# Kernel optimization log

Hardware: AMD Instinct MI355X
Metric: run time of the kernel (lower is better)

The kernel has to match this reference:

```python
import jax, jax.numpy as jnp
import numpy as np

# static config (mirrors init_kwargs)
FS = 512          # frame_seqlen
NFPB = 2          # num_frame_per_block
NIB = 3           # num image/action/state blocks
NAPB = 32         # num_action_per_block
NSPB = 1          # num_state_per_block
LOCAL = 4         # local_attn_size (frames)
FIRST = FS
IMGB = NIB * NFPB * FS
ALEN = NIB * NAPB
SLEN = NIB * NSPB
TOTAL = FIRST + IMGB + ALEN + SLEN   # 3683
DIM = 1536
NH = 12
HD = DIM // NH    # 128
EPS = 1e-6


def _build_mask():
    # faithful port of _visualize_attention_mask (the block-sparse pattern)
    m = np.zeros((TOTAL, TOTAL), dtype=bool)
    fi0, fi1 = 0, FIRST
    ib0, ib1 = fi1, fi1 + IMGB
    a0, a1 = ib1, ib1 + ALEN
    s0 = a1
    m[fi0:fi1, fi0:fi1] = True  # first image: self only (sink)
    for b in range(NIB):
        bs = ib0 + b * NFPB * FS
        be = ib0 + (b + 1) * NFPB * FS
        m[bs:be, fi0:fi1] = True                      # sink
        kv = max(ib0, be - LOCAL * FS)                # local window
        m[bs:be, kv:be] = True
        m[bs:be, a0 + b * NAPB:a0 + (b + 1) * NAPB] = True
        m[bs:be, s0 + b * NSPB:s0 + (b + 1) * NSPB] = True
    for b in range(NIB):
        ab0 = a0 + b * NAPB
        ab1 = a0 + (b + 1) * NAPB
        m[ab0:ab1, fi0:fi1] = True
        ibe = ib0 + (b + 1) * NFPB * FS
        kv = max(ib0, ibe - LOCAL * FS)
        m[ab0:ab1, kv:ibe] = True
        m[ab0:ab1, ab0:ab1] = True
        m[ab0:ab1, s0 + b * NSPB:s0 + (b + 1) * NSPB] = True
    for b in range(NIB):
        ss = s0 + b * NSPB
        se = s0 + (b + 1) * NSPB
        m[ss:se, ss:se] = True
    return m

_MASK = jnp.asarray(_build_mask())


def _rms_norm(x, g):
    # WanRMSNorm over full dim, fp32 accumulation
    v = jnp.mean(jnp.square(x.astype(jnp.float32)), axis=-1, keepdims=True)
    return (x.astype(jnp.float32) * jax.lax.rsqrt(v + EPS)).astype(x.dtype) * g


def _rope(x, cos, sin):
    # x: [B,L,n,hd]; pairs are consecutive (..., hd//2, 2)
    B, L, n, d = x.shape
    xp = x.reshape(B, L, n, d // 2, 2)
    xr, xi = xp[..., 0], xp[..., 1]
    c = cos[None, :, None, :]
    s = sin[None, :, None, :]
    yr = xr * c - xi * s
    yi = xr * s + xi * c
    return jnp.stack([yr, yi], axis=-1).reshape(B, L, n, d)


def setup_inputs() -> dict:
    key = jax.random.key(0)
    ks = jax.random.split(key, 16)
    x = jax.random.normal(ks[0], (1, TOTAL, DIM), jnp.float32)

    def mkfreq(k, L):
        ang = jax.random.uniform(k, (L, HD // 2), jnp.float32, 0.0, 2.0 * np.pi)
        return jnp.stack([jnp.cos(ang), jnp.sin(ang)], axis=-1).reshape(L, HD)

    freqs = mkfreq(ks[1], FIRST + IMGB)
    freqs_action = mkfreq(ks[2], ALEN)
    freqs_state = mkfreq(ks[3], SLEN)
    sc = 1.0 / np.sqrt(DIM)
    Wq = jax.random.normal(ks[4], (DIM, DIM), jnp.float32) * sc
    Wk = jax.random.normal(ks[5], (DIM, DIM), jnp.float32) * sc
    Wv = jax.random.normal(ks[6], (DIM, DIM), jnp.float32) * sc
    Wo = jax.random.normal(ks[7], (DIM, DIM), jnp.float32) * sc
    bq = jax.random.normal(ks[8], (DIM,), jnp.float32) * 0.01
    bk = jax.random.normal(ks[9], (DIM,), jnp.float32) * 0.01
    bv = jax.random.normal(ks[10], (DIM,), jnp.float32) * 0.01
    bo = jax.random.normal(ks[11], (DIM,), jnp.float32) * 0.01
    gq = jnp.ones((DIM,), jnp.float32)
    gk = jnp.ones((DIM,), jnp.float32)
    return {"x": x, "freqs": freqs, "freqs_action": freqs_action,
            "freqs_state": freqs_state, "Wq": Wq, "bq": bq, "Wk": Wk, "bk": bk,
            "Wv": Wv, "bv": bv, "Wo": Wo, "bo": bo, "gq": gq, "gk": gk}


def reference(x, freqs, freqs_action, freqs_state, Wq, bq, Wk, bk, Wv, bv, Wo, bo, gq, gk):
    B, L, _ = x.shape
    q = _rms_norm(x @ Wq + bq, gq).reshape(B, L, NH, HD)
    k = _rms_norm(x @ Wk + bk, gk).reshape(B, L, NH, HD)
    v = (x @ Wv + bv).reshape(B, L, NH, HD)
    # full-sequence rope: image freqs then action freqs then state freqs
    f = jnp.concatenate([freqs, freqs_action, freqs_state], axis=0).reshape(L, HD // 2, 2)
    cos, sin = f[..., 0], f[..., 1]
    q = _rope(q, cos, sin)
    k = _rope(k, cos, sin)
    scores = jnp.einsum('bqnd,bknd->bnqk', q, k) / np.sqrt(HD)
    scores = jnp.where(_MASK[None, None], scores, jnp.finfo(scores.dtype).min)
    p = jax.nn.softmax(scores, axis=-1)
    o = jnp.einsum('bnqk,bknd->bqnd', p, v).reshape(B, L, DIM)
    return o @ Wo + bo
```

## Files before the change

kernel.cpp:

```cpp
#include <hip/hip_runtime.h>

#define LSEQ 3683
#define LPAD 3840
#define DIMSZ 1536
#define NHEAD 12
#define HEADD 128
#define SM_SCALE 0.088388347648318447f

typedef unsigned short u16;
typedef unsigned int u32;
typedef __bf16 bf16x8 __attribute__((ext_vector_type(8)));
typedef float f32x4 __attribute__((ext_vector_type(4)));

__device__ __forceinline__ u16 f2b(float f) {
  u32 u = __float_as_uint(f);
  u += 0x7FFFu + ((u >> 16) & 1u);
  return (u16)(u >> 16);
}
__device__ __forceinline__ float b2f(u16 s) {
  return __uint_as_float(((u32)s) << 16);
}
__device__ __forceinline__ int imax(int a, int b) { return a > b ? a : b; }

__device__ __forceinline__ void gl_lds16(const u16* g, u16* l) {
  __builtin_amdgcn_global_load_lds((const __attribute__((address_space(1))) u32*)g,
                                   (__attribute__((address_space(3))) u32*)l,
                                   16, 0, 0);
}

__device__ __forceinline__ int xcd_swz(int orig, int nwg) {
  int q = nwg >> 3, r = nwg & 7;
  int x = orig & 7, l = orig >> 3;
  return (x < r ? x * (q + 1) : r * (q + 1) + (x - r) * q) + l;
}

__global__ void convert_x_kernel(const float* __restrict__ x, u16* __restrict__ xb) {
  long idx = (long)blockIdx.x * blockDim.x + threadIdx.x;
  long base = idx * 4;
  if (base >= (long)LPAD * DIMSZ) return;
  float4 v;
  if (base < (long)LSEQ * DIMSZ) v = *(const float4*)(x + base);
  else v = make_float4(0.f, 0.f, 0.f, 0.f);
  ushort4 o;
  o.x = f2b(v.x); o.y = f2b(v.y); o.z = f2b(v.z); o.w = f2b(v.w);
  *(ushort4*)(xb + base) = o;
}

__global__ void transpose_w_kernel(const float* __restrict__ W0, const float* __restrict__ W1,
                                   const float* __restrict__ W2, const float* __restrict__ W3,
                                   u16* __restrict__ Wt) {
  const float* W = (blockIdx.z == 0) ? W0 : (blockIdx.z == 1) ? W1 : (blockIdx.z == 2) ? W2 : W3;
  u16* dst = Wt + (size_t)blockIdx.z * DIMSZ * DIMSZ;
  __shared__ float tile[32][33];
  int k0 = blockIdx.x * 32, n0 = blockIdx.y * 32;
  int tx = threadIdx.x & 31, ty = threadIdx.x >> 5;
  #pragma unroll
  for (int i = 0; i < 4; i++) {
    int k = k0 + ty + i * 8;
    tile[ty + i * 8][tx] = W[(size_t)k * DIMSZ + n0 + tx];
  }
  __syncthreads();
  #pragma unroll
  for (int i = 0; i < 4; i++) {
    int n = n0 + ty + i * 8;
    dst[(size_t)n * DIMSZ + k0 + tx] = f2b(tile[tx][ty + i * 8]);
  }
}

#define BAR() __builtin_amdgcn_s_barrier()
#define LGK0() asm volatile("s_waitcnt lgkmcnt(0)" ::: "memory")
#define LGK8() asm volatile("s_waitcnt lgkmcnt(8)" ::: "memory")
#define VMC9() asm volatile("s_waitcnt vmcnt(9)" ::: "memory")
#define VMC6() asm volatile("s_waitcnt vmcnt(6)" ::: "memory")
#define VMC0() asm volatile("s_waitcnt vmcnt(0)" ::: "memory")
#define PRIO1() __builtin_amdgcn_s_setprio(1)
#define PRIO0() __builtin_amdgcn_s_setprio(0)

#define STG_A(buf, q, kt) \
  gl_lds16(gA + (size_t)((q) * 64) * DIMSZ + (kt), &Asg[buf][((q) * 64 + w * 8) * 64]);
#define STG_B(buf, q, kt) \
  gl_lds16(gB + (size_t)((q) * 64) * DIMSZ + (kt), &Bsg[buf][((q) * 64 + w * 8) * 64]);

#define LDA3(buf, mh) { \
  _Pragma("unroll") for (int mf = 0; mf < 3; mf++) { \
    int rb = (wm * 96 + (mh) * 48 + mf * 16) * 64; \
    Ar[mf * 2 + 0] = *(const bf16x8*)&Asg[buf][rb + off0]; \
    Ar[mf * 2 + 1] = *(const bf16x8*)&Asg[buf][rb + off1]; } }
#define LDB3(buf, nh) { \
  _Pragma("unroll") for (int nf = 0; nf < 3; nf++) { \
    int rb = (wn * 96 + (nh) * 48 + nf * 16) * 64; \
    Br[nh][nf * 2 + 0] = *(const bf16x8*)&Bsg[buf][rb + off0]; \
    Br[nh][nf * 2 + 1] = *(const bf16x8*)&Bsg[buf][rb + off1]; } }

#define MFMAQ3(mh, nh) { \
  _Pragma("unroll") for (int mf = 0; mf < 3; mf++) \
    _Pragma("unroll") for (int nf = 0; nf < 3; nf++) { \
      acc[(mh)*3+mf][(nh)*3+nf] = __builtin_amdgcn_mfma_f32_16x16x32_bf16(Ar[mf*2+0], Br[nh][nf*2+0], acc[(mh)*3+mf][(nh)*3+nf], 0, 0, 0); \
      acc[(mh)*3+mf][(nh)*3+nf] = __builtin_amdgcn_mfma_f32_16x16x32_bf16(Ar[mf*2+1], Br[nh][nf*2+1], acc[(mh)*3+mf][(nh)*3+nf], 0, 0, 0); } }

__launch_bounds__(512, 2)
__global__ void gemm_qkv384_kernel(const u16* __restrict__ A, const u16* __restrict__ Wt,
                                   const float* __restrict__ bq, const float* __restrict__ bk,
                                   const float* __restrict__ bv,
                                   u16* __restrict__ Qb, u16* __restrict__ Kb,
                                   u16* __restrict__ Vt) {
  __shared__ __align__(16) u16 Asg[2][384 * 64];
  __shared__ __align__(16) u16 Bsg[2][192 * 64];

  int wg = xcd_swz(blockIdx.x, 10 * 24);
  int nt = wg % 24;
  int m0 = (wg / 24) * 384;
  int which = nt >> 3;
  const float* bias = (which == 0) ? bq : (which == 1) ? bk : bv;

  int t = threadIdx.x;
  int lane = t & 63, w = t >> 6;
  int c = lane & 15, g = lane >> 4;
  int wm = w >> 1, wn = w & 1;

  int srow = t >> 3;
  int schunk = ((t & 7) ^ (srow & 7)) * 8;
  const u16* gA = A + (size_t)(m0 + srow) * DIMSZ + schunk;
  const u16* gB = Wt + (size_t)(nt * 192 + srow) * DIMSZ + schunk;

  int off0 = c * 64 + ((g) ^ (c & 7)) * 8;
  int off1 = c * 64 + ((g + 4) ^ (c & 7)) * 8;

  f32x4 acc[6][6];
  f32x4 zero = {0.f, 0.f, 0.f, 0.f};
  #pragma unroll
  for (int am = 0; am < 6; am++)
    #pragma unroll
    for (int an = 0; an < 6; an++) acc[am][an] = zero;
  bf16x8 Ar[6];
  bf16x8 Br[2][6];

  STG_B(0, 0, 0) STG_B(0, 1, 0) STG_B(0, 2, 0)
  STG_A(0, 0, 0) STG_A(0, 1, 0) STG_A(0, 2, 0)
  STG_A(0, 3, 0) STG_A(0, 4, 0) STG_A(0, 5, 0)
  STG_B(1, 0, 64) STG_B(1, 1, 64) STG_B(1, 2, 64)
  STG_A(1, 0, 64) STG_A(1, 1, 64) STG_A(1, 2, 64)
  STG_A(1, 3, 64) STG_A(1, 4, 64) STG_A(1, 5, 64)
  VMC9();
  BAR();

  for (int i = 0; i < DIMSZ / 64 / 2 - 1; ++i) {
    int kt2 = (2 * i + 2) * 64;
    int kt3 = (2 * i + 3) * 64;
    LDA3(0, 0) LDB3(0, 0)
    LGK8(); BAR(); LGK0();
    PRIO1(); MFMAQ3(0, 0) PRIO0();
    BAR();
    LDB3(0, 1)
    BAR(); LGK0();
    PRIO1(); MFMAQ3(0, 1) PRIO0();
    BAR();
    LDA3(0, 1)
    STG_B(0, 0, kt2) STG_B(0, 1, kt2) STG_B(0, 2, kt2)
    BAR(); LGK0();
    PRIO1(); MFMAQ3(1, 1) PRIO0();
    BAR();
    STG_A(0, 0, kt2) STG_A(0, 1, kt2) STG_A(0, 2, kt2)
    VMC6(); BAR();
    PRIO1(); MFMAQ3(1, 0) PRIO0();
    BAR();
    LDA3(1, 0) LDB3(1, 0)
    STG_A(0, 3, kt2) STG_A(0, 4, kt2) STG_A(0, 5, kt2)
    LGK8(); BAR(); LGK0();
    PRIO1(); MFMAQ3(0, 0) PRIO0();
    BAR();
    LDB3(1, 1)
    BAR(); LGK0();
    PRIO1(); MFMAQ3(0, 1) PRIO0();
    BAR();
    LDA3(1, 1)
    STG_B(1, 0, kt3) STG_B(1, 1, kt3) STG_B(1, 2, kt3)
    BAR(); LGK0();
    PRIO1(); MFMAQ3(1, 1) PRIO0();
    BAR();
    STG_A(1, 0, kt3) STG_A(1, 1, kt3) STG_A(1, 2, kt3)
    STG_A(1, 3, kt3) STG_A(1, 4, kt3) STG_A(1, 5, kt3)
    VMC9(); BAR();
    PRIO1(); MFMAQ3(1, 0) PRIO0();
    BAR();
  }

  {
    LDA3(0, 0) LDB3(0, 0)
    LGK8(); BAR(); LGK0();
    PRIO1(); MFMAQ3(0, 0) PRIO0();
    BAR();
    LDB3(0, 1)
    BAR(); LGK0();
    PRIO1(); MFMAQ3(0, 1) PRIO0();
    BAR();
    LDA3(0, 1)
    BAR(); LGK0();
    PRIO1(); MFMAQ3(1, 1) PRIO0();
    BAR();
    VMC0(); BAR();
    PRIO1(); MFMAQ3(1, 0) PRIO0();
    BAR();
    LDA3(1, 0) LDB3(1, 0)
    LGK8(); BAR(); LGK0();
    PRIO1(); MFMAQ3(0, 0) PRIO0();
    BAR();
    LDB3(1, 1)
    BAR(); LGK0();
    PRIO1(); MFMAQ3(0, 1) PRIO0();
    BAR();
    LDA3(1, 1)
    BAR(); LGK0();
    PRIO1(); MFMAQ3(1, 1) PRIO0();
    MFMAQ3(1, 0)
  }

  #pragma unroll
  for (int an = 0; an < 6; an++) {
    int ncol = (nt & 7) * 192 + wn * 96 + (an / 3) * 48 + (an % 3) * 16 + c;
    float bvv = bias[ncol];
    #pragma unroll
    for (int am = 0; am < 6; am++) {
      int rowb = m0 + wm * 96 + (am / 3) * 48 + (am % 3) * 16 + 4 * g;
      if (which == 2) {
        ushort4 pv;
        pv.x = f2b(acc[am][an][0] + bvv);
        pv.y = f2b(acc[am][an][1] + bvv);
        pv.z = f2b(acc[am][an][2] + bvv);
        pv.w = f2b(acc[am][an][3] + bvv);
        *(ushort4*)&Vt[(size_t)ncol * LPAD + rowb] = pv;
      } else {
        u16* P = (which == 1) ? Kb : Qb;
        #pragma unroll
        for (int r = 0; r < 4; r++)
          P[(size_t)(rowb + r) * DIMSZ + ncol] = f2b(acc[am][an][r] + bvv);
      }
    }
  }
}

#define GEMM_PROLOGUE()                                                          \
  __shared__ __align__(16) u16 As[4][128 * 32];                                  \
  __shared__ __align__(16) u16 Bs[4][128 * 32];                                  \
  int t = threadIdx.x;                                                           \
  int lane = t & 63, w = t >> 6;                                                 \
  int g = lane >> 4, c = lane & 15;                                              \
  int wm = w >> 1, wn = w & 1;                                                   \
  f32x4 acc[4][4];                                                               \
  f32x4 zero = {0.f, 0.f, 0.f, 0.f};                                             \
  _Pragma("unroll") for (int fr = 0; fr < 4; fr++)                               \
      _Pragma("unroll") for (int fc = 0; fc < 4; fc++) acc[fr][fc] = zero;       \
  int srcc = (((lane & 3) ^ ((lane >> 2) & 3))) * 8;    \
  const u16* gA = A + (size_t)(m0 + w * 32 + (lane >> 2)) * DIMSZ + srcc;        \
  const u16* gB = Bt + (size_t)(n0 + w * 32 + (lane >> 2)) * DIMSZ + srcc;       \
  int gsw = (g ^ (c & 3)) * 8;

#define GEMM_STAGE(buf, kt)                                                      \
  _Pragma("unroll") for (int q = 0; q < 2; q++) {                                \
    gl_lds16(gA + (size_t)(q * 16) * DIMSZ + (kt), &As[buf][(w * 32 + q * 16) * 32]); \
    gl_lds16(gB + (size_t)(q * 16) * DIMSZ + (kt), &Bs[buf][(w * 32 + q * 16) * 32]); \
  }

#define GEMM_COMPUTE(buf)                                                        \
  {                                                                              \
    bf16x8 af[4], bfr[4];                                                        \
    _Pragma("unroll") for (int fr = 0; fr < 4; fr++)                             \
        af[fr] = *(const bf16x8*)&As[buf][(wm * 64 + fr * 16 + c) * 32 + gsw];   \
    _Pragma("unroll") for (int fc = 0; fc < 4; fc++)                             \
        bfr[fc] = *(const bf16x8*)&Bs[buf][(wn * 64 + fc * 16 + c) * 32 + gsw];  \
    _Pragma("unroll") for (int fr = 0; fr < 4; fr++)                             \
        _Pragma("unroll") for (int fc = 0; fc < 4; fc++)                         \
            acc[fr][fc] = __builtin_amdgcn_mfma_f32_16x16x32_bf16(af[fr], bfr[fc], acc[fr][fc], 0, 0, 0); \
  }

#define GEMM_MAINLOOP()                                                          \
  GEMM_STAGE(0, 0)                                                               \
  GEMM_STAGE(1, 32)                                                              \
  GEMM_STAGE(2, 64)                                                              \
  {                                                                              \
    const int nk = DIMSZ / 32;                                                   \
    for (int ki = 0; ki < nk; ki++) {                                            \
      int rem = nk - ki;                                                         \
      if (rem > 2)      asm volatile("s_waitcnt vmcnt(8)" ::: "memory");         \
      else if (rem == 2) asm volatile("s_waitcnt vmcnt(4)" ::: "memory");        \
      else               asm volatile("s_waitcnt vmcnt(0)" ::: "memory");        \
      __builtin_amdgcn_s_barrier();                                              \
      if (ki + 3 < nk) { GEMM_STAGE((ki + 3) & 3, (ki + 3) * 32) }               \
      GEMM_COMPUTE(ki & 3)                                                       \
    }                                                                            \
  }

__launch_bounds__(256)
__global__ void gemm_out_kernel(const u16* __restrict__ A, const u16* __restrict__ Bt,
                                const float* __restrict__ bias, float* __restrict__ outF) {
  int wg = xcd_swz(blockIdx.x, 29 * 12);
  int n0 = (wg % 12) * 128;
  int m0 = (wg / 12) * 128;

  GEMM_PROLOGUE()
  GEMM_MAINLOOP()

  #pragma unroll
  for (int fc = 0; fc < 4; fc++) {
    int col = n0 + wn * 64 + fc * 16 + c;
    float bvv = bias[col];
    #pragma unroll
    for (int fr = 0; fr < 4; fr++) {
      int rowb = m0 + wm * 64 + fr * 16 + 4 * g;
      #pragma unroll
      for (int r = 0; r < 4; r++) {
        int row = rowb + r;
        if (row < LSEQ) outF[(size_t)row * DIMSZ + col] = acc[fr][fc][r] + bvv;
      }
    }
  }
}

__launch_bounds__(256)
__global__ void normrope_kernel(u16* __restrict__ Qb, u16* __restrict__ Kb,
                                const float* __restrict__ gq, const float* __restrict__ gk,
                                const float* __restrict__ freqs, const float* __restrict__ freqs_a,
                                const float* __restrict__ freqs_s) {
  int l = blockIdx.x;
  int sel = blockIdx.y;
  u16* P = sel ? Kb : Qb;
  const float* gvec = sel ? gk : gq;
  int t = threadIdx.x;
  u16* row = P + (size_t)l * DIMSZ;
  float xv[6];
  #pragma unroll
  for (int i = 0; i < 3; i++) {
    int p = i * 256 + t;
    ushort2 u = *(const ushort2*)(row + 2 * p);
    xv[2 * i] = b2f(u.x);
    xv[2 * i + 1] = b2f(u.y);
  }
  float ss = 0.f;
  #pragma unroll
  for (int i = 0; i < 6; i++) ss += xv[i] * xv[i];
  #pragma unroll
  for (int d = 32; d; d >>= 1) ss += __shfl_down(ss, d);
  __shared__ float red[4];
  __shared__ float rshare;
  if ((t & 63) == 0) red[t >> 6] = ss;
  __syncthreads();
  if (t == 0) rshare = rsqrtf((red[0] + red[1] + red[2] + red[3]) * (1.0f / DIMSZ) + 1e-6f);
  __syncthreads();
  float rms = rshare;

  const float* f = (l < 3584) ? (freqs + (size_t)l * HEADD)
                : (l < 3680) ? (freqs_a + (size_t)(l - 3584) * HEADD)
                             : (freqs_s + (size_t)(l - 3680) * HEADD);
  #pragma unroll
  for (int i = 0; i < 3; i++) {
    int p = i * 256 + t;
    int j = p & 63;
    float2 csn = *(const float2*)(f + 2 * j);
    float2 gv = *(const float2*)(gvec + 2 * p);
    float xr = xv[2 * i] * rms * gv.x;
    float xi = xv[2 * i + 1] * rms * gv.y;
    ushort2 o;
    o.x = f2b(xr * csn.x - xi * csn.y);
    o.y = f2b(xr * csn.y + xi * csn.x);
    *(ushort2*)(row + 2 * p) = o;
  }
}

#define PSLOT_U16 16640
__launch_bounds__(256, 2)
__global__ void attn_dense_kernel(const u16* __restrict__ Q, const u16* __restrict__ K,
                                  const u16* __restrict__ Vt, u16* __restrict__ O,
                                  u16* __restrict__ DP) {
  __shared__ __align__(16) u16 Ks[2][32 * 144];
  __shared__ __align__(16) u16 Vs[2][128 * 40];
  __shared__ __align__(16) u16 Pl[4][32 * 40];

  int bx = blockIdx.x;
  int qbase, h, part, nparts, fb;
  if (bx < 48) { qbase = (bx / 12) * 128; h = bx % 12; part = 0; nparts = 1; fb = -1; }
  else if (bx < 336) { int i = bx - 48; int qb = i / 36; h = (i / 3) % 12; part = i % 3; nparts = 3; fb = 0; qbase = 512 + qb * 128; }
  else if (bx < 720) { int i = bx - 336; int qb = i / 48; h = (i / 4) % 12; part = i % 4; nparts = 4; fb = 1; qbase = 1536 + qb * 128; }
  else { int i = bx - 720; int qb = i / 48; h = (i / 4) % 12; part = i % 4; nparts = 4; fb = 2; qbase = 2560 + qb * 128; }

  int S0, E0, S1, E1, S2, E2, S3, E3, niv;
  if (fb < 0) { S0 = 0; E0 = 512; S1 = E1 = S2 = E2 = S3 = E3 = 0; niv = 1; }
  else {
    int be = 512 + (fb + 1) * 1024;
    int kv = imax(512, be - 2048);
    S0 = 0; E0 = 512; S1 = kv; E1 = be;
    S2 = 3584 + 32 * fb; E2 = S2 + 32; S3 = 3680 + fb; E3 = S3 + 1; niv = 4;
  }
  int B0 = S0 & ~31, B1 = S1 & ~31, B2 = S2 & ~31, B3 = S3 & ~31;
  int T1 = (E0 - B0 + 31) >> 5;
  int T2 = T1 + ((niv > 1) ? ((E1 - B1 + 31) >> 5) : 0);
  int T3 = T2 + ((niv > 2) ? ((E2 - B2 + 31) >> 5) : 0);
  int T4 = T3 + ((niv > 3) ? ((E3 - B3 + 31) >> 5) : 0);
  int ntile = T4;
  int rlo = (ntile * part) / nparts, rhi = (ntile * (part + 1)) / nparts;

  auto tile_of = [&](int f, int& k0, int& lo, int& hi) {
    k0 = B0 + (f << 5); lo = S0; hi = E0;
    if (niv > 1 && f >= T1) { k0 = B1 + ((f - T1) << 5); lo = S1; hi = E1; }
    if (niv > 2 && f >= T2) { k0 = B2 + ((f - T2) << 5); lo = S2; hi = E2; }
    if (niv > 3 && f >= T3) { k0 = B3 + ((f - T3) << 5); lo = S3; hi = E3; }
  };

  int T = threadIdx.x;
  int lane = T & 63, w = T >> 6, g = lane >> 4, c = lane & 15;

  const u16* kgp = K + (size_t)(T >> 3) * DIMSZ + h * HEADD + 8 * (T & 7);
  int kds = (T >> 3) * 144 + 8 * (T & 7);
  const u16* vgp = Vt + ((size_t)h * HEADD + (T >> 1)) * LPAD + 16 * (T & 1);
  int vds = (T >> 1) * 40 + 16 * (T & 1);

  uint4 sk0, sk1, sv0, sv1;
  auto stage_load = [&](int k0) {
    const u16* kp = kgp + (size_t)k0 * DIMSZ;
    sk0 = *(const uint4*)(kp);
    sk1 = *(const uint4*)(kp + 64);
    sv0 = *(const uint4*)(vgp + k0);
    sv1 = *(const uint4*)(vgp + k0 + 8);
  };
  auto stage_write = [&](int buf) {
    *(uint4*)&Ks[buf][kds] = sk0;
    *(uint4*)&Ks[buf][kds + 64] = sk1;
    *(uint4*)&Vs[buf][vds] = sv0;
    *(uint4*)&Vs[buf][vds + 8] = sv1;
  };

  int qrow0 = qbase + 32 * w;
  bf16x8 qf[2][4];
  #pragma unroll
  for (int a = 0; a < 2; a++) {
    const u16* qp = Q + (size_t)(qrow0 + a * 16 + c) * DIMSZ + h * HEADD + 8 * g;
    #pragma unroll
    for (int s = 0; s < 4; s++) qf[a][s] = *(const bf16x8*)(qp + 32 * s);
  }

  f32x4 zero = {0.f, 0.f, 0.f, 0.f};
  f32x4 acc[2][8];
  f32x4 lacc[2];
  #pragma unroll
  for (int a = 0; a < 2; a++) {
    lacc[a] = zero;
    #pragma unroll
    for (int cc = 0; cc < 8; cc++) acc[a][cc] = zero;
  }
  bf16x8 onesv;
  {
    u16 ob = 0x3F80;
    #pragma unroll
    for (int i = 0; i < 8; i++) onesv[i] = ((const __bf16*)&ob)[0];
  }

  u16* Pw = &Pl[w][0];
  const float c1 = SM_SCALE * 1.44269504088896340f;
  const float c2 = 12.0f * 1.44269504088896340f;

  {
    int k0, lo, hi; tile_of(rlo, k0, lo, hi);
    stage_load(k0);
    stage_write(0);
  }
  __syncthreads();
  int cur = 0;

  for (int t = rlo; t < rhi; ++t) {
    int ck0, clo, chi; tile_of(t, ck0, clo, chi);
    bool pre = (t + 1 < rhi);
    if (pre) { int nk0, nl, nh; tile_of(t + 1, nk0, nl, nh); stage_load(nk0); }

    f32x4 sc[2][2];
    sc[0][0] = zero; sc[0][1] = zero; sc[1][0] = zero; sc[1][1] = zero;
    #pragma unroll
    for (int k2 = 0; k2 < 2; k2++)
      #pragma unroll
      for (int s = 0; s < 4; s++) {
        bf16x8 kf = *(const bf16x8*)&Ks[cur][(16 * k2 + c) * 144 + 32 * s + 8 * g];
        sc[0][k2] = __builtin_amdgcn_mfma_f32_16x16x32_bf16(qf[0][s], kf, sc[0][k2], 0, 0, 0);
        sc[1][k2] = __builtin_amdgcn_mfma_f32_16x16x32_bf16(qf[1][s], kf, sc[1][k2], 0, 0, 0);
      }

    #pragma unroll
    for (int a = 0; a < 2; a++)
      #pragma unroll
      for (int k2 = 0; k2 < 2; k2++) {
        int k = ck0 + k2 * 16 + c;
        bool valid = (k >= clo) && (k < chi);
        #pragma unroll
        for (int r = 0; r < 4; r++) {
          float p = exp2f(sc[a][k2][r] * c1 - c2);
          Pw[(a * 16 + 4 * g + r) * 40 + k2 * 16 + c] = valid ? f2b(p) : (u16)0;
        }
      }
    asm volatile("s_waitcnt lgkmcnt(0)" ::: "memory");
    __builtin_amdgcn_sched_barrier(0);

    bf16x8 pa0 = *(const bf16x8*)&Pw[c * 40 + 8 * g];
    bf16x8 pa1 = *(const bf16x8*)&Pw[(16 + c) * 40 + 8 * g];

    #pragma unroll
    for (int cc = 0; cc < 8; cc++) {
      bf16x8 vf = *(const bf16x8*)&Vs[cur][(cc * 16 + c) * 40 + 8 * g];
      acc[0][cc] = __builtin_amdgcn_mfma_f32_16x16x32_bf16(pa0, vf, acc[0][cc], 0, 0, 0);
      acc[1][cc] = __builtin_amdgcn_mfma_f32_16x16x32_bf16(pa1, vf, acc[1][cc], 0, 0, 0);
    }
    lacc[0] = __builtin_amdgcn_mfma_f32_16x16x32_bf16(pa0, onesv, lacc[0], 0, 0, 0);
    lacc[1] = __builtin_amdgcn_mfma_f32_16x16x32_bf16(pa1, onesv, lacc[1], 0, 0, 0);

    if (pre) stage_write(cur ^ 1);
    __syncthreads();
    cur ^= 1;
  }

  if (nparts == 1) {
    float inv[2][4];
    #pragma unroll
    for (int a = 0; a < 2; a++)
      #pragma unroll
      for (int r = 0; r < 4; r++) inv[a][r] = (lacc[a][r] > 0.f) ? 1.0f / lacc[a][r] : 0.f;
    #pragma unroll
    for (int a = 0; a < 2; a++)
      #pragma unroll
      for (int cc = 0; cc < 8; cc++)
        #pragma unroll
        for (int r = 0; r < 4; r++) {
          int row = qrow0 + a * 16 + 4 * g + r;
          O[(size_t)row * DIMSZ + h * HEADD + cc * 16 + c] = f2b(acc[a][cc][r] * inv[a][r]);
        }
  } else {
    int qb = (qbase - 512 - fb * 1024) >> 7;
    int sbase = (fb == 0) ? 0 : (fb == 1 ? 288 : 672);
    int slot = sbase + (qb * 12 + h) * nparts + part;
    u16* DPs = DP + (size_t)slot * PSLOT_U16;
    float* lout = (float*)(DPs + 16384);
    #pragma unroll
    for (int a = 0; a < 2; a++) {
      #pragma unroll
      for (int cc = 0; cc < 8; cc++)
        #pragma unroll
        for (int r = 0; r < 4; r++)
          DPs[(32 * w + a * 16 + 4 * g + r) * 128 + cc * 16 + c] = f2b(acc[a][cc][r]);
      if (c == 0)
        #pragma unroll
        for (int r = 0; r < 4; r++) lout[32 * w + a * 16 + 4 * g + r] = lacc[a][r];
    }
  }
}

__launch_bounds__(256)
__global__ void attn_merge_dense(const u16* __restrict__ DP, u16* __restrict__ O) {
  int qi = blockIdx.x, h = blockIdx.y;
  int fb = qi >> 3, qb = qi & 7;
  int nparts = (fb == 0) ? 3 : 4;
  int sbase = (fb == 0) ? 0 : (fb == 1 ? 288 : 672);
  int slot0 = sbase + (qb * 12 + h) * nparts;
  int qbase = 512 + fb * 1024 + qb * 128;
  int T = threadIdx.x;
  int row = T >> 1, c0 = 64 * (T & 1);

  float sum[64];
  #pragma unroll
  for (int j = 0; j < 64; j++) sum[j] = 0.f;
  float l = 0.f;
  for (int p = 0; p < nparts; p++) {
    const u16* S = DP + (size_t)(slot0 + p) * PSLOT_U16;
    l += ((const float*)(S + 16384))[row];
    #pragma unroll
    for (int j = 0; j < 64; j += 8) {
      uint4 v = *(const uint4*)&S[row * 128 + c0 + j];
      const u16* pv = (const u16*)&v;
      #pragma unroll
      for (int q = 0; q < 8; q++) sum[j + q] += b2f(pv[q]);
    }
  }
  float inv = (l > 0.f) ? 1.0f / l : 0.f;
  u16 tmp[64];
  #pragma unroll
  for (int j = 0; j < 64; j++) tmp[j] = f2b(sum[j] * inv);
  u16* op = O + (size_t)(qbase + row) * DIMSZ + h * HEADD + c0;
  #pragma unroll
  for (int j = 0; j < 64; j += 8) *(uint4*)(op + j) = *(uint4*)&tmp[j];
}

__launch_bounds__(256, 2)
__global__ void attn_tail_kernel(const u16* __restrict__ Q, const u16* __restrict__ K,
                                 const u16* __restrict__ Vt, u16* __restrict__ O,
                                 float* __restrict__ Part) {
  __shared__ __align__(16) char smem[20608];
  __shared__ float Lsum[32];

  int bx = blockIdx.x;
  int h = blockIdx.y;
  int qt, part;
  if (bx < 3) { qt = 112 + bx; part = 0; }
  else if (bx < 6) { qt = 112 + (bx - 3); part = 1; }
  else { qt = 115; part = 0; }
  int qbase = qt * 32;
  bool heavy = (qt <= 114);

  int t = threadIdx.x, lane = t & 63, w = t >> 6, g = lane >> 4, c = lane & 15;

  int S0, E0, S1, E1, S2, E2, S3, E3, niv;
  if (qbase < 3680) {
    int b = (qbase - 3584) >> 5;
    int ibe = 512 + (b + 1) * 1024;
    int kv = imax(512, ibe - 2048);
    S0 = 0; E0 = 512; S1 = kv; E1 = ibe;
    S2 = 3584 + 32 * b; E2 = S2 + 32; S3 = 3680 + b; E3 = S3 + 1; niv = 4;
  } else {
    S0 = 3680; E0 = 3683; S1 = S2 = S3 = 0; E1 = E2 = E3 = 0; niv = 1;
  }
  bool diag = (qbase >= 3680);

  int B0 = S0 & ~31, B1 = S1 & ~31, B2 = S2 & ~31, B3 = S3 & ~31;
  int T1 = (E0 - B0 + 31) >> 5;
  int T2 = T1 + ((niv > 1) ? ((E1 - B1 + 31) >> 5) : 0);
  int T3 = T2 + ((niv > 2) ? ((E2 - B2 + 31) >> 5) : 0);
  int T4 = T3 + ((niv > 3) ? ((E3 - B3 + 31) >> 5) : 0);
  int ntile = T4;

  int rlo = 0, rhi = ntile;
  if (heavy) { int half = (ntile + 1) >> 1; if (part == 0) rhi = half; else rlo = half; }

  auto tile_of = [&](int f, int& k0, int& lo, int& hi) {
    k0 = B0 + (f << 5); lo = S0; hi = E0;
    if (niv > 1 && f >= T1) { k0 = B1 + ((f - T1) << 5); lo = S1; hi = E1; }
    if (niv > 2 && f >= T2) { k0 = B2 + ((f - T2) << 5); lo = S2; hi = E2; }
    if (niv > 3 && f >= T3) { k0 = B3 + ((f - T3) << 5); lo = S3; hi = E3; }
  };

  bf16x8 qf[2][4];
  #pragma unroll
  for (int a = 0; a < 2; a++) {
    const u16* qp = Q + (size_t)(qbase + a * 16 + c) * DIMSZ + h * HEADD + 8 * g;
    #pragma unroll
    for (int s = 0; s < 4; s++) qf[a][s] = *(const bf16x8*)(qp + 32 * s);
  }

  f32x4 zero = {0.f, 0.f, 0.f, 0.f};
  f32x4 acc[2][8];
  f32x4 lacc[2];
  #pragma unroll
  for (int a = 0; a < 2; a++) {
    lacc[a] = zero;
    #pragma unroll
    for (int cc = 0; cc < 8; cc++) acc[a][cc] = zero;
  }
  bf16x8 onesv;
  {
    u16 ob = 0x3F80;
    #pragma unroll
    for (int i = 0; i < 8; i++) onesv[i] = ((const __bf16*)&ob)[0];
  }

  u16* PwA = (u16*)smem + w * 2560;
  u16* PwB = PwA + 1280;

  bf16x8 kc[2][4], vbuf[8], pa0, pa1;
  const float c1 = SM_SCALE * 1.44269504088896340f;
  const float c2 = 12.0f * 1.44269504088896340f;

  auto loadK = [&](int k0) {
    #pragma unroll
    for (int k2 = 0; k2 < 2; k2++) {
      const u16* kp = K + (size_t)(k0 + 16 * k2 + c) * DIMSZ + h * HEADD + 8 * g;
      #pragma unroll
      for (int s = 0; s < 4; s++) kc[k2][s] = *(const bf16x8*)(kp + 32 * s);
    }
  };
  auto loadV = [&](int k0) {
    #pragma unroll
    for (int cc = 0; cc < 8; cc++)
      vbuf[cc] = *(const bf16x8*)(Vt + (size_t)(h * HEADD + cc * 16 + c) * LPAD + k0 + 8 * g);
  };
  auto QKf = [&](f32x4 (&sc)[2][2]) {
    sc[0][0] = zero; sc[0][1] = zero; sc[1][0] = zero; sc[1][1] = zero;
    #pragma unroll
    for (int k2 = 0; k2 < 2; k2++)
      #pragma unroll
      for (int s = 0; s < 4; s++) {
        sc[0][k2] = __builtin_amdgcn_mfma_f32_16x16x32_bf16(qf[0][s], kc[k2][s], sc[0][k2], 0, 0, 0);
        sc[1][k2] = __builtin_amdgcn_mfma_f32_16x16x32_bf16(qf[1][s], kc[k2][s], sc[1][k2], 0, 0, 0);
      }
  };
  auto smstore = [&](f32x4 (&sc)[2][2], int k0, int lo, int hi, u16* Pw) {
    #pragma unroll
    for (int a = 0; a < 2; a++)
      #pragma unroll
      for (int k2 = 0; k2 < 2; k2++) {
        int k = k0 + k2 * 16 + c;
        bool valid = (k >= lo) && (k < hi);
        #pragma unroll
        for (int r = 0; r < 4; r++) {
          float p = exp2f(sc[a][k2][r] * c1 - c2);
          bool v = valid;
          if (diag) { int qr = qbase + a * 16 + 4 * g + r; v = v && (k == qr); }
          Pw[(a * 16 + 4 * g + r) * 40 + k2 * 16 + c] = v ? f2b(p) : (u16)0;
        }
      }
  };
  auto readP = [&](u16* Pw) {
    pa0 = *(const bf16x8*)&Pw[c * 40 + 8 * g];
    pa1 = *(const bf16x8*)&Pw[(16 + c) * 40 + 8 * g];
  };
  auto PV = [&]() {
    #pragma unroll
    for (int cc = 0; cc < 8; cc++) {
      acc[0][cc] = __builtin_amdgcn_mfma_f32_16x16x32_bf16(pa0, vbuf[cc], acc[0][cc], 0, 0, 0);
      acc[1][cc] = __builtin_amdgcn_mfma_f32_16x16x32_bf16(pa1, vbuf[cc], acc[1][cc], 0, 0, 0);
    }
    lacc[0] = __builtin_amdgcn_mfma_f32_16x16x32_bf16(pa0, onesv, lacc[0], 0, 0, 0);
    lacc[1] = __builtin_amdgcn_mfma_f32_16x16x32_bf16(pa1, onesv, lacc[1], 0, 0, 0);
  };

  int i = rlo + w;
  if (i < rhi) {
    int ik0, ilo, ihi; tile_of(i, ik0, ilo, ihi);
    loadK(ik0);
    loadV(ik0);
    {
      f32x4 sc[2][2]; QKf(sc);
      smstore(sc, ik0, ilo, ihi, PwA);
    }
    asm volatile("s_waitcnt lgkmcnt(0)" ::: "memory");
    __builtin_amdgcn_sched_barrier(0);
    readP(PwA);
    int nx = i + 4;
    int nk0 = 0, nlo = 0, nhi = 0;
    bool useB = true;
    if (nx < rhi) { tile_of(nx, nk0, nlo, nhi); loadK(nk0); }
    while (nx < rhi) {
      int ck0 = nk0, clo = nlo, chi = nhi;
      f32x4 sc[2][2]; QKf(sc);
      int nn = nx + 4;
      if (nn < rhi) { tile_of(nn, nk0, nlo, nhi); loadK(nk0); }
      u16* Pw = useB ? PwB : PwA;
      smstore(sc, ck0, clo, chi, Pw);
      PV();
      loadV(ck0);
      asm volatile("s_waitcnt lgkmcnt(0)" ::: "memory");
      __builtin_amdgcn_sched_barrier(0);
      readP(Pw);
      useB = !useB;
      i = nx; nx = nn;
    }
    PV();
  }

  __syncthreads();
  float* Oacc = (float*)smem;
  if (w == 0) {
    #pragma unroll
    for (int a = 0; a < 2; a++) {
      #pragma unroll
      for (int cc = 0; cc < 8; cc++)
        #pragma unroll
        for (int r = 0; r < 4; r++)
          Oacc[(a * 16 + 4 * g + r) * 132 + cc * 16 + c] = acc[a][cc][r];
      if (c == 0)
        #pragma unroll
        for (int r = 0; r < 4; r++) Lsum[a * 16 + 4 * g + r] = lacc[a][r];
    }
  }
  __syncthreads();
  #pragma unroll
  for (int ww = 1; ww < 4; ww++) {
    if (w == ww) {
      #pragma unroll
      for (int a = 0; a < 2; a++) {
        #pragma unroll
        for (int cc = 0; cc < 8; cc++)
          #pragma unroll
          for (int r = 0; r < 4; r++)
            Oacc[(a * 16 + 4 * g + r) * 132 + cc * 16 + c] += acc[a][cc][r];
        if (c == 0)
          #pragma unroll
          for (int r = 0; r < 4; r++) Lsum[a * 16 + 4 * g + r] += lacc[a][r];
      }
    }
    __syncthreads();
  }

  int row = t >> 3, c0 = (t & 7) * 16;
  if (heavy) {
    size_t slot = ((size_t)((qt - 112) * 12 + h)) * 2 + part;
    float* P = Part + slot * 4160;
    #pragma unroll
    for (int j = 0; j < 16; j += 4)
      *(float4*)&P[row * 128 + c0 + j] = *(float4*)&Oacc[row * 132 + c0 + j];
    if ((t & 7) == 0) P[4096 + row] = Lsum[row];
  } else {
    int orow = qbase + row;
    if (orow < LSEQ) {
      float lsv = Lsum[row];
      float inv = (lsv > 0.f) ? 1.0f / lsv : 0.f;
      u16 tmp[16];
      #pragma unroll
      for (int j = 0; j < 16; j++) tmp[j] = f2b(Oacc[row * 132 + c0 + j] * inv);
      u16* op = O + (size_t)orow * DIMSZ + h * HEADD + c0;
      *(uint4*)(op) = *(uint4*)&tmp[0];
      *(uint4*)(op + 8) = *(uint4*)&tmp[8];
    }
  }
}

__launch_bounds__(256)
__global__ void attn_merge_tail(const float* __restrict__ Part, u16* __restrict__ O) {
  int b = blockIdx.x, h = blockIdx.y;
  const float* A = Part + ((size_t)(b * 12 + h)) * 2 * 4160;
  const float* B = A + 4160;
  int t = threadIdx.x;
  int row = t >> 3, c0 = (t & 7) * 16;
  float l = A[4096 + row] + B[4096 + row];
  float inv = (l > 0.f) ? 1.0f / l : 0.f;
  int orow = 3584 + b * 32 + row;
  u16 tmp[16];
  #pragma unroll
  for (int jj = 0; jj < 16; jj += 4) {
    float4 va = *(const float4*)&A[row * 128 + c0 + jj];
    float4 vb = *(const float4*)&B[row * 128 + c0 + jj];
    tmp[jj + 0] = f2b((va.x + vb.x) * inv);
    tmp[jj + 1] = f2b((va.y + vb.y) * inv);
    tmp[jj + 2] = f2b((va.z + vb.z) * inv);
    tmp[jj + 3] = f2b((va.w + vb.w) * inv);
  }
  u16* op = O + (size_t)orow * DIMSZ + h * HEADD + c0;
  *(uint4*)(op) = *(uint4*)&tmp[0];
  *(uint4*)(op + 8) = *(uint4*)&tmp[8];
}

extern "C" void kernel_launch(void* const* d_in, const int* in_sizes, int n_in,
                              void* d_out, int out_size, void* d_ws, size_t ws_size,
                              hipStream_t stream) {
  (void)in_sizes; (void)n_in; (void)out_size; (void)ws_size;
  const float* x       = (const float*)d_in[0];
  const float* freqs   = (const float*)d_in[1];
  const float* freqs_a = (const float*)d_in[2];
  const float* freqs_s = (const float*)d_in[3];
  const float* Wq = (const float*)d_in[4];
  const float* bq = (const float*)d_in[5];
  const float* Wk = (const float*)d_in[6];
  const float* bk = (const float*)d_in[7];
  const float* Wv = (const float*)d_in[8];
  const float* bv = (const float*)d_in[9];
  const float* Wo = (const float*)d_in[10];
  const float* bo = (const float*)d_in[11];
  const float* gq = (const float*)d_in[12];
  const float* gk = (const float*)d_in[13];
  float* out = (float*)d_out;

  char* ws = (char*)d_ws;
  size_t off = 0;
  auto alloc = [&](size_t bytes) -> void* {
    void* p = ws + off;
    off += (bytes + 255) & ~(size_t)255;
    return p;
  };
  u16* xb   = (u16*)alloc((size_t)LPAD * DIMSZ * 2);
  u16* Wt   = (u16*)alloc((size_t)4 * DIMSZ * DIMSZ * 2);
  u16* Qb   = (u16*)alloc((size_t)LPAD * DIMSZ * 2);
  u16* Kb   = (u16*)alloc((size_t)LPAD * DIMSZ * 2);
  u16* Vt   = (u16*)alloc((size_t)DIMSZ * LPAD * 2);
  u16* Ob   = (u16*)alloc((size_t)LPAD * DIMSZ * 2);
  u16* DP   = (u16*)alloc((size_t)1056 * PSLOT_U16 * 2);
  float* PartT = (float*)alloc((size_t)3 * 12 * 2 * 4160 * 4);

  convert_x_kernel<<<(LPAD * DIMSZ / 4 + 255) / 256, 256, 0, stream>>>(x, xb);
  transpose_w_kernel<<<dim3(48, 48, 4), 256, 0, stream>>>(Wq, Wk, Wv, Wo, Wt);

  gemm_qkv384_kernel<<<dim3(240), 512, 0, stream>>>(xb, Wt, bq, bk, bv, Qb, Kb, Vt);

  normrope_kernel<<<dim3(LSEQ, 2), 256, 0, stream>>>(Qb, Kb, gq, gk, freqs, freqs_a, freqs_s);

  attn_dense_kernel<<<dim3(1104), 256, 0, stream>>>(Qb, Kb, Vt, Ob, DP);
  attn_tail_kernel<<<dim3(7, 12), 256, 0, stream>>>(Qb, Kb, Vt, Ob, PartT);
  attn_merge_dense<<<dim3(24, 12), 256, 0, stream>>>(DP, Ob);
  attn_merge_tail<<<dim3(3, 12), 256, 0, stream>>>(PartT, Ob);

  gemm_out_kernel<<<dim3(29 * 12), 256, 0, stream>>>(Ob, Wt + 3 * (size_t)DIMSZ * DIMSZ, bo, out);
}
```

Baseline: 256.6 us.

## Widen attention blocks to 256 queries, swizzle K LDS, and reduce split-K partitions

The dense attention kernel now uses 512-thread blocks, each covering 256 query rows with 8 waves, so every staged K/V tile is reused across twice as many queries. The key-split count per block drops (3→2 and 4→3), and the partial-result slots and merge kernel are resized to match. The padded K LDS layout is replaced by an XOR swizzle to avoid bank conflicts without padding. A mask-free fast path skips per-element validity checks on full tiles and uses the hardware exp2. The grid shrinks from 1104 to 408 blocks, which may hurt load balance across CUs, and the larger blocks raise register pressure under the new launch bounds.

```diff
diff --git a/kernel.cpp b/kernel.cpp
--- a/kernel.cpp
+++ b/kernel.cpp
@@ -366,21 +366,21 @@
   }
 }
 
-#define PSLOT_U16 16640
-__launch_bounds__(256, 2)
+#define PSLOT2_U16 33280
+__launch_bounds__(512, 4)
 __global__ void attn_dense_kernel(const u16* __restrict__ Q, const u16* __restrict__ K,
                                   const u16* __restrict__ Vt, u16* __restrict__ O,
                                   u16* __restrict__ DP) {
-  __shared__ __align__(16) u16 Ks[2][32 * 144];
+  __shared__ __align__(16) u16 Ks[2][32 * 128];
   __shared__ __align__(16) u16 Vs[2][128 * 40];
-  __shared__ __align__(16) u16 Pl[4][32 * 40];
+  __shared__ __align__(16) u16 Pl[8][32 * 40];
 
   int bx = blockIdx.x;
   int qbase, h, part, nparts, fb;
-  if (bx < 48) { qbase = (bx / 12) * 128; h = bx % 12; part = 0; nparts = 1; fb = -1; }
-  else if (bx < 336) { int i = bx - 48; int qb = i / 36; h = (i / 3) % 12; part = i % 3; nparts = 3; fb = 0; qbase = 512 + qb * 128; }
-  else if (bx < 720) { int i = bx - 336; int qb = i / 48; h = (i / 4) % 12; part = i % 4; nparts = 4; fb = 1; qbase = 1536 + qb * 128; }
-  else { int i = bx - 720; int qb = i / 48; h = (i / 4) % 12; part = i % 4; nparts = 4; fb = 2; qbase = 2560 + qb * 128; }
+  if (bx < 24) { qbase = (bx / 12) * 256; h = bx % 12; part = 0; nparts = 1; fb = -1; }
+  else if (bx < 120) { int i = bx - 24; int qb = i / 24; h = (i / 2) % 12; part = i % 2; nparts = 2; fb = 0; qbase = 512 + qb * 256; }
+  else if (bx < 264) { int i = bx - 120; int qb = i / 36; h = (i / 3) % 12; part = i % 3; nparts = 3; fb = 1; qbase = 1536 + qb * 256; }
+  else { int i = bx - 264; int qb = i / 36; h = (i / 3) % 12; part = i % 3; nparts = 3; fb = 2; qbase = 2560 + qb * 256; }
 
   int S0, E0, S1, E1, S2, E2, S3, E3, niv;
   if (fb < 0) { S0 = 0; E0 = 512; S1 = E1 = S2 = E2 = S3 = E3 = 0; niv = 1; }
@@ -408,24 +408,21 @@
   int T = threadIdx.x;
   int lane = T & 63, w = T >> 6, g = lane >> 4, c = lane & 15;
 
-  const u16* kgp = K + (size_t)(T >> 3) * DIMSZ + h * HEADD + 8 * (T & 7);
-  int kds = (T >> 3) * 144 + 8 * (T & 7);
-  const u16* vgp = Vt + ((size_t)h * HEADD + (T >> 1)) * LPAD + 16 * (T & 1);
-  int vds = (T >> 1) * 40 + 16 * (T & 1);
-
-  uint4 sk0, sk1, sv0, sv1;
+  int krow = T >> 4, kch = T & 15;
+  const u16* kgp = K + (size_t)krow * DIMSZ + h * HEADD + 8 * kch;
+  int kds = krow * 128 + ((kch & 8) | ((kch & 7) ^ (krow & 7))) * 8;
+  int vrow = T >> 2, vp4 = T & 3;
+  const u16* vgp = Vt + ((size_t)h * HEADD + vrow) * LPAD + 8 * vp4;
+  int vds = vrow * 40 + 8 * vp4;
+
+  uint4 sk, sv;
   auto stage_load = [&](int k0) {
-    const u16* kp = kgp + (size_t)k0 * DIMSZ;
-    sk0 = *(const uint4*)(kp);
-    sk1 = *(const uint4*)(kp + 64);
-    sv0 = *(const uint4*)(vgp + k0);
-    sv1 = *(const uint4*)(vgp + k0 + 8);
+    sk = *(const uint4*)(kgp + (size_t)k0 * DIMSZ);
+    sv = *(const uint4*)(vgp + k0);
   };
   auto stage_write = [&](int buf) {
-    *(uint4*)&Ks[buf][kds] = sk0;
-    *(uint4*)&Ks[buf][kds + 64] = sk1;
-    *(uint4*)&Vs[buf][vds] = sv0;
-    *(uint4*)&Vs[buf][vds + 8] = sv1;
+    *(uint4*)&Ks[buf][kds] = sk;
+    *(uint4*)&Vs[buf][vds] = sv;
   };
 
   int qrow0 = qbase + 32 * w;
@@ -476,23 +473,35 @@
     for (int k2 = 0; k2 < 2; k2++)
       #pragma unroll
       for (int s = 0; s < 4; s++) {
-        bf16x8 kf = *(const bf16x8*)&Ks[cur][(16 * k2 + c) * 144 + 32 * s + 8 * g];
+        bf16x8 kf = *(const bf16x8*)&Ks[cur][(16 * k2 + c) * 128 + ((4 * s + g) ^ (c & 7)) * 8];
         sc[0][k2] = __builtin_amdgcn_mfma_f32_16x16x32_bf16(qf[0][s], kf, sc[0][k2], 0, 0, 0);
         sc[1][k2] = __builtin_amdgcn_mfma_f32_16x16x32_bf16(qf[1][s], kf, sc[1][k2], 0, 0, 0);
       }
 
-    #pragma unroll
-    for (int a = 0; a < 2; a++)
-      #pragma unroll
-      for (int k2 = 0; k2 < 2; k2++) {
-        int k = ck0 + k2 * 16 + c;
-        bool valid = (k >= clo) && (k < chi);
-        #pragma unroll
-        for (int r = 0; r < 4; r++) {
-          float p = exp2f(sc[a][k2][r] * c1 - c2);
-          Pw[(a * 16 + 4 * g + r) * 40 + k2 * 16 + c] = valid ? f2b(p) : (u16)0;
+    if (ck0 >= clo && ck0 + 32 <= chi) {
+      #pragma unroll
+      for (int a = 0; a < 2; a++)
+        #pragma unroll
+        for (int k2 = 0; k2 < 2; k2++)
+          #pragma unroll
+          for (int r = 0; r < 4; r++) {
+            float p = __builtin_amdgcn_exp2f(sc[a][k2][r] * c1 - c2);
+            Pw[(a * 16 + 4 * g + r) * 40 + k2 * 16 + c] = f2b(p);
+          }
+    } else {
+      #pragma unroll
+      for (int a = 0; a < 2; a++)
+        #pragma unroll
+        for (int k2 = 0; k2 < 2; k2++) {
+          int k = ck0 + k2 * 16 + c;
+          bool valid = (k >= clo) && (k < chi);
+          #pragma unroll
+          for (int r = 0; r < 4; r++) {
+            float p = __builtin_amdgcn_exp2f(sc[a][k2][r] * c1 - c2);
+            Pw[(a * 16 + 4 * g + r) * 40 + k2 * 16 + c] = valid ? f2b(p) : (u16)0;
+          }
         }
-      }
+    }
     asm volatile("s_waitcnt lgkmcnt(0)" ::: "memory");
     __builtin_amdgcn_sched_barrier(0);
 
@@ -529,11 +538,11 @@
           O[(size_t)row * DIMSZ + h * HEADD + cc * 16 + c] = f2b(acc[a][cc][r] * inv[a][r]);
         }
   } else {
-    int qb = (qbase - 512 - fb * 1024) >> 7;
-    int sbase = (fb == 0) ? 0 : (fb == 1 ? 288 : 672);
+    int qb = (qbase - 512 - fb * 1024) >> 8;
+    int sbase = (fb == 0) ? 0 : (fb == 1 ? 96 : 240);
     int slot = sbase + (qb * 12 + h) * nparts + part;
-    u16* DPs = DP + (size_t)slot * PSLOT_U16;
-    float* lout = (float*)(DPs + 16384);
+    u16* DPs = DP + (size_t)slot * PSLOT2_U16;
+    float* lout = (float*)(DPs + 32768);
     #pragma unroll
     for (int a = 0; a < 2; a++) {
       #pragma unroll
@@ -551,24 +560,26 @@
 __launch_bounds__(256)
 __global__ void attn_merge_dense(const u16* __restrict__ DP, u16* __restrict__ O) {
   int qi = blockIdx.x, h = blockIdx.y;
-  int fb = qi >> 3, qb = qi & 7;
-  int nparts = (fb == 0) ? 3 : 4;
-  int sbase = (fb == 0) ? 0 : (fb == 1 ? 288 : 672);
+  int fb = qi >> 3, qb128 = qi & 7;
+  int qb = qb128 >> 1, half = qb128 & 1;
+  int nparts = (fb == 0) ? 2 : 3;
+  int sbase = (fb == 0) ? 0 : (fb == 1 ? 96 : 240);
   int slot0 = sbase + (qb * 12 + h) * nparts;
-  int qbase = 512 + fb * 1024 + qb * 128;
+  int qbase = 512 + fb * 1024 + qb128 * 128;
   int T = threadIdx.x;
   int row = T >> 1, c0 = 64 * (T & 1);
+  int srow = half * 128 + row;
 
   float sum[64];
   #pragma unroll
   for (int j = 0; j < 64; j++) sum[j] = 0.f;
   float l = 0.f;
   for (int p = 0; p < nparts; p++) {
-    const u16* S = DP + (size_t)(slot0 + p) * PSLOT_U16;
-    l += ((const float*)(S + 16384))[row];
+    const u16* S = DP + (size_t)(slot0 + p) * PSLOT2_U16;
+    l += ((const float*)(S + 32768))[srow];
     #pragma unroll
     for (int j = 0; j < 64; j += 8) {
-      uint4 v = *(const uint4*)&S[row * 128 + c0 + j];
+      uint4 v = *(const uint4*)&S[srow * 128 + c0 + j];
       const u16* pv = (const u16*)&v;
       #pragma unroll
       for (int q = 0; q < 8; q++) sum[j + q] += b2f(pv[q]);
@@ -863,7 +874,7 @@
   u16* Kb   = (u16*)alloc((size_t)LPAD * DIMSZ * 2);
   u16* Vt   = (u16*)alloc((size_t)DIMSZ * LPAD * 2);
   u16* Ob   = (u16*)alloc((size_t)LPAD * DIMSZ * 2);
-  u16* DP   = (u16*)alloc((size_t)1056 * PSLOT_U16 * 2);
+  u16* DP   = (u16*)alloc((size_t)384 * PSLOT2_U16 * 2);
   float* PartT = (float*)alloc((size_t)3 * 12 * 2 * 4160 * 4);
 
   convert_x_kernel<<<(LPAD * DIMSZ / 4 + 255) / 256, 256, 0, stream>>>(x, xb);
@@ -873,7 +884,7 @@
 
   normrope_kernel<<<dim3(LSEQ, 2), 256, 0, stream>>>(Qb, Kb, gq, gk, freqs, freqs_a, freqs_s);
 
-  attn_dense_kernel<<<dim3(1104), 256, 0, stream>>>(Qb, Kb, Vt, Ob, DP);
+  attn_dense_kernel<<<dim3(408), 512, 0, stream>>>(Qb, Kb, Vt, Ob, DP);
   attn_tail_kernel<<<dim3(7, 12), 256, 0, stream>>>(Qb, Kb, Vt, Ob, PartT);
   attn_merge_dense<<<dim3(24, 12), 256, 0, stream>>>(DP, Ob);
   attn_merge_tail<<<dim3(3, 12), 256, 0, stream>>>(PartT, Ob);
```

After: 304.6 us. 18.7% more time.
